# Kernel optimization log

Measured on AMD Instinct MI355X. Metric: run time of the kernel, lower is better.

The kernel has to match this reference:

```python
import jax, jax.numpy as jnp
import numpy as np

B, L, D, N_LAYERS = 128, 256, 512, 6
NEG = -9e15  # -9000000000000000.0 in the torch source


def _pair_coef(a1, L, D):
    # Faithful reduction of the torch repeat_interleave(dim=2) construction:
    # first half of a_input satisfies a_input[b, i, j, m] = h[b, i, (j*D + m)//L],
    # so sum_m a_input[...,m]*a1[m] = h[b,i] . c[j] with
    # c[j, f] = sum_{m : (j*D+m)//L == f} a1[m].
    j = jnp.arange(L)[:, None]
    m = jnp.arange(D)[None, :]
    idx = (j * D + m) // L  # [L, D], values in [0, D-1]
    c = jnp.zeros((L, D), a1.dtype)
    c = c.at[jnp.arange(L)[:, None], idx].add(jnp.broadcast_to(a1[None, :], (L, D)))
    return c


def gat_layer(x, adj, W, a):
    # h = x @ W; e[b,i,j] = relu(a_input[b,i,j,:] @ a)  (relu overwrites leakyrelu in source)
    h = x @ W  # [B, L, D]
    d = W.shape[1]
    a1, a2 = a[:d, 0], a[d:, 0]
    c = _pair_coef(a1, h.shape[1], d)  # [L, D]
    e = jax.nn.relu(jnp.einsum('bif,jf->bij', h, c) + (h @ a2)[:, None, :])
    att = jnp.where(adj > 0, e, NEG)
    att = jax.nn.softmax(att, axis=2)  # dropout is identity in eval
    h_prime = jnp.einsum('bij,bjd->bid', att, h)
    return jax.nn.elu(h_prime)  # concat=True branch


def position_weight(x, left_len, aspect_len, text_len):
    j = jnp.arange(x.shape[1])[None, :].astype(jnp.float32)  # [1, L]
    l = left_len[:, None].astype(jnp.float32)
    r = (left_len + aspect_len - 1)[:, None].astype(jnp.float32)
    tl = text_len[:, None].astype(jnp.float32)
    ctx = (text_len - aspect_len)[:, None].astype(jnp.float32)
    w = jnp.where(j < l, 1.0 - (l - j) / ctx,
        jnp.where(j <= r, 0.0,
        jnp.where(j < tl, 1.0 - (j - r) / ctx, 0.0)))
    return w[..., None].astype(x.dtype) * x


def aspect_mask(x, left_len, aspect_len):
    j = jnp.arange(x.shape[1])[None, :]
    l = left_len[:, None]
    r = (left_len + aspect_len - 1)[:, None]
    m = ((j >= l) & (j <= r)).astype(x.dtype)
    return m[..., None] * x


def setup_inputs() -> dict:
    key = jax.random.key(0)
    ks = jax.random.split(key, 6)
    x = jax.random.normal(ks[0], (B, L, D), jnp.float32)
    adj = jax.random.randint(ks[1], (B, L, L), 0, 2, jnp.int32)
    adj = adj.at[:, jnp.arange(L), jnp.arange(L)].set(1)  # self loops
    left_len = jax.random.randint(ks[2], (B,), 0, 20, jnp.int32)
    aspect_len = jax.random.randint(ks[3], (B,), 1, 6, jnp.int32)
    text_len = jnp.full((B,), L, jnp.int32)
    W_stack = jax.random.normal(ks[4], (N_LAYERS, D, D), jnp.float32) * (1.414 / np.sqrt(D))
    a_stack = jax.random.normal(ks[5], (N_LAYERS, 2 * D, 1), jnp.float32) * 0.05
    return {"x": x, "W_stack": W_stack, "a_stack": a_stack, "adj": adj,
            "left_len": left_len, "aspect_len": aspect_len, "text_len": text_len}


def reference(x, W_stack, a_stack, adj, left_len, aspect_len, text_len):
    text_out = x
    xp = position_weight(text_out, left_len, aspect_len, text_len)
    h1 = jax.nn.relu(gat_layer(xp, adj, W_stack[0], a_stack[0]))
    h1 = position_weight(h1, left_len, aspect_len, text_len)
    x_graph = jnp.zeros_like(h1)
    for i in range(1, N_LAYERS):
        x_graph = x_graph + jax.nn.relu(gat_layer(h1, adj, W_stack[i], a_stack[i]))
    x_graph = 0.2 * x_graph
    graph_mask = aspect_mask(x_graph, left_len, aspect_len)
    # hop == 1 attention pooling
    alpha_mat = jnp.einsum('bld,bmd->blm', graph_mask, text_out)  # [B, L, L]
    alpha = jax.nn.softmax(alpha_mat.sum(axis=1, keepdims=True), axis=2)  # [B, 1, L]
    a1 = jnp.einsum('blm,bmd->bld', alpha, text_out)[:, 0, :]  # [B, D]
    return a1
```

## Files before the change

kernel.cpp:

```cpp
#include <hip/hip_runtime.h>

#define NB 128
#define NLQ 256
#define ND 512
#define NLAYERS 6
#define DD (ND*ND)
#define MN (1024*ND)
#define HTB 131072

typedef _Float16 f16x8 __attribute__((ext_vector_type(8)));
typedef __fp16 fp16x2 __attribute__((ext_vector_type(2)));
typedef _Float16 f16x4v __attribute__((ext_vector_type(4)));
typedef float f32x4 __attribute__((ext_vector_type(4)));
typedef unsigned int u32x2 __attribute__((ext_vector_type(2)));
typedef unsigned int u32x4 __attribute__((ext_vector_type(4)));
typedef unsigned short ushort_t;

#define GLOAD16(gp, lp) __builtin_amdgcn_global_load_lds( \
    (const __attribute__((address_space(1))) void*)(gp), \
    (__attribute__((address_space(3))) void*)(lp), 16, 0, 0)

__device__ __forceinline__ float wave_max(float v){
  #pragma unroll
  for(int off=32; off; off>>=1) v = fmaxf(v, __shfl_xor(v, off));
  return v;
}
__device__ __forceinline__ float wave_sum(float v){
  #pragma unroll
  for(int off=32; off; off>>=1) v += __shfl_xor(v, off);
  return v;
}
__device__ __forceinline__ unsigned int pk16(float a, float b){
  fp16x2 h = __builtin_amdgcn_cvt_pkrtz(a, b);
  return __builtin_bit_cast(unsigned int, h);
}

__global__ __launch_bounds__(256) void k_scal(const float* __restrict__ a_stack,
                                              float* __restrict__ scal){
  int layer = blockIdx.x;
  const float* a = a_stack + (size_t)layer*2*ND;
  int t = threadIdx.x;
  float v0 = a[t];
  float v1 = a[256 + t];
  v0 = wave_sum(v0); v1 = wave_sum(v1);
  __shared__ float s0[4], s1[4];
  int wave = t>>6, lane = t&63;
  if(lane==0){ s0[wave]=v0; s1[wave]=v1; }
  __syncthreads();
  if(t==0){
    scal[layer*2+0] = s0[0]+s0[1]+s0[2]+s0[3];
    scal[layer*2+1] = s1[0]+s1[1]+s1[2]+s1[3];
  }
}

__global__ __launch_bounds__(256) void k_wa2(const float* __restrict__ Wst,
                                             const float* __restrict__ ast,
                                             float* __restrict__ v){
  int l  = blockIdx.x >> 7;
  int rg = blockIdx.x & 127;
  int i  = rg*4 + (threadIdx.x>>6);
  int lane = threadIdx.x & 63;
  const float4* wr = (const float4*)(Wst + (size_t)(l+1)*DD + (size_t)i*ND);
  const float4* ar = (const float4*)(ast + (size_t)(l+1)*2*ND + ND);
  float4 w0=wr[lane], w1=wr[lane+64], a0=ar[lane], a1=ar[lane+64];
  float d = w0.x*a0.x + w0.y*a0.y + w0.z*a0.z + w0.w*a0.w
          + w1.x*a1.x + w1.y*a1.y + w1.z*a1.z + w1.w*a1.w;
  d = wave_sum(d);
  if(lane==0) v[l*ND + i] = d;
}

__global__ __launch_bounds__(256) void k_wcvt(const float* __restrict__ Wsrc,
                                              ushort_t* __restrict__ Ho){
  __shared__ float CT[64][65];
  int bid = blockIdx.x;
  int l  = bid >> 6;
  int kt = (bid >> 3) & 7, nt = bid & 7;
  const float* Wl = Wsrc + (size_t)l*DD;
  int t = threadIdx.x;
  int r = t >> 2, c4 = (t&3)*16;
  #pragma unroll
  for(int u=0;u<4;u++){
    float4 vv = *(const float4*)(Wl + (size_t)(kt*64+r)*ND + nt*64 + c4 + u*4);
    CT[r][c4+u*4+0]=vv.x; CT[r][c4+u*4+1]=vv.y;
    CT[r][c4+u*4+2]=vv.z; CT[r][c4+u*4+3]=vv.w;
  }
  __syncthreads();
  int n = t >> 2, kc = t & 3;
  unsigned int o[8];
  #pragma unroll
  for(int j=0;j<8;j++)
    o[j] = pk16(CT[kc*16 + 2*j][n], CT[kc*16 + 2*j + 1][n]);
  ushort_t* dh = Ho + (size_t)l*DD + (size_t)(nt*64+n)*ND + kt*64 + kc*16;
  *(u32x4*)(dh)     = (u32x4){o[0],o[1],o[2],o[3]};
  *(u32x4*)(dh + 8) = (u32x4){o[4],o[5],o[6],o[7]};
}

#define ROWB 80
template<int MODE>
__device__ __forceinline__ void gemm_tile(const float* __restrict__ A,
                                          const ushort_t* __restrict__ Wth,
                                          float* __restrict__ C,
                                          unsigned int* __restrict__ hP,
                                          ushort_t* __restrict__ Pbuf,
                                          float* __restrict__ tp4,
                                          const float* __restrict__ a2,
                                          const float* __restrict__ scal,
                                          const int* __restrict__ left,
                                          const int* __restrict__ asp,
                                          const int* __restrict__ tl,
                                          int mtile, int ntile, unsigned char* lds){
  unsigned char* Ah = lds;
  unsigned char* Bh = lds + 128*ROWB;

  int t = threadIdx.x;
  int m0 = mtile*128, n0 = ntile*128;
  int lane = t & 63, wid = t >> 6;
  int wr = wid >> 1, wc = wid & 1;
  int lrow = lane & 15, kb = lane >> 4;

  f32x4 acc[4][4];
  #pragma unroll
  for(int mi=0;mi<4;mi++)
    #pragma unroll
    for(int ni=0;ni<4;ni++)
      acc[mi][ni] = (f32x4){0.f,0.f,0.f,0.f};

  int a_row = t >> 3;
  int a_kq  = t & 7;
  int w_n   = t >> 2;
  int w_kc  = t & 3;

  float wgt_[4] = {1.f,1.f,1.f,1.f};
  if(MODE == 1){
    int b = mtile >> 1;
    float lf=(float)left[b], aspf=(float)asp[b], tlf=(float)tl[b];
    float rr=lf+aspf-1.f, ctx=tlf-aspf;
    #pragma unroll
    for(int p=0;p<4;p++){
      float jf = (float)((mtile&1)*128 + a_row + p*32);
      float w;
      if(jf < lf)       w = 1.f-(lf-jf)/ctx;
      else if(jf <= rr) w = 0.f;
      else if(jf < tlf) w = 1.f-(jf-rr)/ctx;
      else              w = 0.f;
      wgt_[p] = w;
    }
  }

  float4 pa[4];
  u32x4 pwh[2];

  #pragma unroll
  for(int p=0;p<4;p++)
    pa[p] = *(const float4*)(A + (size_t)(m0 + a_row + p*32)*ND + a_kq*4);
  #pragma unroll
  for(int h=0;h<2;h++)
    pwh[h] = *(const u32x4*)(Wth + (size_t)(n0 + w_n + h*64)*ND + w_kc*8);

  for(int k0=0; k0<ND; k0+=32){
    #pragma unroll
    for(int p=0;p<4;p++){
      int row = a_row + p*32;
      unsigned int c0 = pk16(pa[p].x*wgt_[p], pa[p].y*wgt_[p]);
      unsigned int c1 = pk16(pa[p].z*wgt_[p], pa[p].w*wgt_[p]);
      *(u32x2*)(Ah + row*ROWB + a_kq*8) = (u32x2){c0, c1};
    }
    #pragma unroll
    for(int h=0;h<2;h++)
      *(u32x4*)(Bh + (w_n + h*64)*ROWB + w_kc*16) = pwh[h];
    __syncthreads();

    if(k0 + 32 < ND){
      int kn = k0 + 32;
      #pragma unroll
      for(int p=0;p<4;p++)
        pa[p] = *(const float4*)(A + (size_t)(m0 + a_row + p*32)*ND + kn + a_kq*4);
      #pragma unroll
      for(int h=0;h<2;h++)
        pwh[h] = *(const u32x4*)(Wth + (size_t)(n0 + w_n + h*64)*ND + kn + w_kc*8);
    }

    f16x8 ah[4], bh[4];
    #pragma unroll
    for(int mi=0;mi<4;mi++)
      ah[mi] = *(const f16x8*)(Ah + (wr*64 + mi*16 + lrow)*ROWB + kb*16);
    #pragma unroll
    for(int ni=0;ni<4;ni++)
      bh[ni] = *(const f16x8*)(Bh + (wc*64 + ni*16 + lrow)*ROWB + kb*16);

    #pragma unroll
    for(int mi=0;mi<4;mi++)
      #pragma unroll
      for(int ni=0;ni<4;ni++)
        acc[mi][ni] = __builtin_amdgcn_mfma_f32_16x16x32_f16(ah[mi], bh[ni], acc[mi][ni], 0,0,0);
    __syncthreads();
  }

  int rg = lane >> 4;
  int cc = lane & 15;
  if(MODE == 0){
    #pragma unroll
    for(int mi=0;mi<4;mi++)
      #pragma unroll
      for(int ni=0;ni<4;ni++){
        int col = n0 + wc*64 + ni*16 + cc;
        #pragma unroll
        for(int q=0;q<4;q++){
          int row = m0 + wr*64 + mi*16 + rg*4 + q;
          C[(size_t)row*ND + col] = acc[mi][ni][q];
        }
      }
  } else {
    float S0 = scal[0], S1 = scal[1];
    float* CT = (float*)lds;
    int b = m0 >> 8;
    int ibase = m0 & 255;
    int tr   = t >> 1;
    int tch  = t & 1;
    float tpsum = 0.f;
    #pragma unroll
    for(int p=0;p<2;p++){
      if(wc == p){
        #pragma unroll
        for(int mi=0;mi<4;mi++)
          #pragma unroll
          for(int ni=0;ni<4;ni++)
            #pragma unroll
            for(int q=0;q<4;q++)
              CT[(ni*16+cc)*130 + wr*64 + mi*16 + rg*4 + q] = acc[mi][ni][q];
      }
      __syncthreads();
      int lcol = t >> 6;
      int lrow2 = (t & 63)*2;
      #pragma unroll
      for(int u=0;u<16;u++){
        int c = lcol + u*4;
        float2 v2 = *(float2*)&CT[c*130 + lrow2];
        size_t uidx = ((size_t)b*HTB + (size_t)(n0 + p*64 + c)*256 + ibase + lrow2) >> 1;
        hP[uidx] = pk16(v2.x, v2.y);
      }
      {
        int cpr = t & 31;
        int rq  = t >> 5;
        #pragma unroll
        for(int rr2=0; rr2<16; rr2++){
          int row = rq*16 + rr2;
          float pval = S0*CT[(2*cpr)*130 + row] + S1*CT[(2*cpr+1)*130 + row];
          int ig = ibase + row;
          _Float16 ph = (_Float16)pval;
          size_t addr = (size_t)b*262144 + (size_t)(ig>>5)*32768
                      + (size_t)(ig&31)*256 + (n0>>1) + p*32 + cpr;
          Pbuf[addr] = __builtin_bit_cast(unsigned short, ph);
        }
      }
      #pragma unroll 8
      for(int cc2=0; cc2<32; cc2++){
        int c = tch*32 + cc2;
        tpsum = fmaf(CT[c*130 + tr], a2[n0 + p*64 + c], tpsum);
      }
      __syncthreads();
    }
    tpsum += __shfl_xor(tpsum, 1);
    if(tch == 0) tp4[(n0>>7)*32768 + m0 + tr] = tpsum;
  }
}

__global__ __launch_bounds__(256) void k_gemm_t(const float* __restrict__ A,
                                                const ushort_t* __restrict__ Wth,
                                                unsigned int* __restrict__ hP,
                                                ushort_t* __restrict__ Pbuf,
                                                float* __restrict__ tp4,
                                                const float* __restrict__ a2,
                                                const float* __restrict__ scal,
                                                const int* __restrict__ left,
                                                const int* __restrict__ asp,
                                                const int* __restrict__ tl){
  __shared__ unsigned char lds[33280];
  int bid = blockIdx.x;
  int ntile = (bid >> 3) & 3;
  int mtile = (bid & 7) | ((bid >> 5) << 3);
  gemm_tile<1>(A, Wth, nullptr, hP, Pbuf, tp4, a2, scal, left, asp, tl,
               mtile, ntile, lds);
}

__global__ __launch_bounds__(256) void k_gemm_b(const float* __restrict__ Abase, long aStride,
                                                const ushort_t* __restrict__ Wth,
                                                float* __restrict__ Cbase){
  __shared__ unsigned char lds[2*128*ROWB];
  int l  = blockIdx.x >> 5;
  int tb = blockIdx.x & 31;
  gemm_tile<0>(Abase + (size_t)l*aStride, Wth + (size_t)l*DD,
               Cbase + (size_t)l*MN, nullptr, nullptr, nullptr,
               nullptr, nullptr, nullptr, nullptr, nullptr, tb>>2, tb&3, lds);
}

__global__ __launch_bounds__(256) void k_attn0(
    const ushort_t* __restrict__ hTH,
    const int* __restrict__ adj,
    const float* __restrict__ tpart,
    const int* __restrict__ left, const int* __restrict__ asp, const int* __restrict__ tl,
    float* __restrict__ PA){
  __shared__ unsigned char attH[32*512];
  __shared__ unsigned char BsH[16384];

  int bid = blockIdx.x;
  int b  = bid & 127;
  int ic = bid >> 7;
  int i0 = ic*32;
  int tid = threadIdx.x;
  int lane = tid & 63, w = tid >> 6;
  const ushort_t* HH = hTH + (size_t)b*HTB;
  const ushort_t* Pt = (const ushort_t*)PA + (size_t)b*262144 + (size_t)ic*32768;

  float t0v=0.f, t1v=0.f, t2v=0.f, t3v=0.f;
  #pragma unroll
  for(int nt=0; nt<4; nt++){
    float4 tv = ((const float4*)(tpart + nt*32768 + b*256))[lane];
    t0v += tv.x; t1v += tv.y; t2v += tv.z; t3v += tv.w;
  }

  for(int rr=0; rr<8; rr++){
    int il = w*8 + rr;
    int i  = i0 + il;
    f16x4v pv = *(const f16x4v*)(Pt + il*256 + lane*4);
    int4 av = ((const int4*)(adj + ((size_t)b*NLQ + i)*NLQ))[lane];
    float e0 = fmaxf((float)pv[0] + t0v, 0.f);
    float e1 = fmaxf((float)pv[1] + t1v, 0.f);
    float e2 = fmaxf((float)pv[2] + t2v, 0.f);
    float e3 = fmaxf((float)pv[3] + t3v, 0.f);
    float m = -3.0e38f;
    if(av.x>0) m = e0;
    if(av.y>0) m = fmaxf(m, e1);
    if(av.z>0) m = fmaxf(m, e2);
    if(av.w>0) m = fmaxf(m, e3);
    m = wave_max(m);
    float p0 = (av.x>0) ? __expf(e0-m) : 0.f;
    float p1 = (av.y>0) ? __expf(e1-m) : 0.f;
    float p2 = (av.z>0) ? __expf(e2-m) : 0.f;
    float p3 = (av.w>0) ? __expf(e3-m) : 0.f;
    float s = wave_sum(p0+p1+p2+p3);
    float inv = 1.f/s;
    unsigned int w0 = pk16(p0*inv, p1*inv);
    unsigned int w1 = pk16(p2*inv, p3*inv);
    int off = il*512 + ((lane*8) ^ ((il&7)<<4));
    *(u32x2*)(attH + off) = (u32x2){w0,w1};
  }

  int wm = w >> 1, wn = w & 1;
  int lrow = lane & 15, kb = lane >> 4;
  int rg = lane >> 4, cc = lane & 15;
  float lf=(float)left[b], aspf=(float)asp[b], tlf=(float)tl[b];
  float rrv=lf+aspf-1.f, ctx=tlf-aspf;
  int arow = wm*16 + lrow;
  int aswz = (arow&7)<<4;

  for(int dp=0; dp<2; dp++){
    int d0 = dp*256;
    f32x4 acc[8];
    #pragma unroll
    for(int ni=0;ni<8;ni++) acc[ni] = (f32x4){0.f,0.f,0.f,0.f};
    for(int ks=0; ks<8; ks++){
      int j0 = ks*32;
      __syncthreads();
      #pragma unroll
      for(int u=0;u<4;u++){
        int chunk = (u*4 + w)*64 + lane;
        int row = chunk >> 2, sl = chunk & 3;
        GLOAD16(HH + (size_t)(d0+row)*256 + j0 + sl*8, BsH + (u*4+w)*1024);
      }
      __syncthreads();
      int aoff = arow*512 + ((j0*2 + kb*16) ^ aswz);
      f16x8 ah = *(const f16x8*)(attH + aoff);
      #pragma unroll
      for(int ni=0; ni<8; ni++){
        f16x8 bh = *(const f16x8*)(BsH + (wn*128 + ni*16 + lrow)*64 + kb*16);
        acc[ni] = __builtin_amdgcn_mfma_f32_16x16x32_f16(ah, bh, acc[ni], 0,0,0);
      }
    }
    #pragma unroll
    for(int q=0;q<4;q++){
      int row = i0 + wm*16 + rg*4 + q;
      float fi = (float)row;
      float wgt;
      if(fi < lf)        wgt = 1.f-(lf-fi)/ctx;
      else if(fi <= rrv) wgt = 0.f;
      else if(fi < tlf)  wgt = 1.f-(fi-rrv)/ctx;
      else               wgt = 0.f;
      #pragma unroll
      for(int ni=0;ni<8;ni++){
        int col = d0 + wn*128 + ni*16 + cc;
        PA[((size_t)b*NLQ + row)*ND + col] = wgt*fmaxf(acc[ni][q], 0.f);
      }
    }
  }
}

__global__ __launch_bounds__(256) void k_tv(const float* __restrict__ h1,
                                            const float* __restrict__ v,
                                            float* __restrict__ T){
  int row  = blockIdx.x*4 + (threadIdx.x>>6);
  int lane = threadIdx.x & 63;
  const float4* hr = (const float4*)(h1 + (size_t)row*ND);
  float4 h0 = hr[lane], h1v = hr[lane+64];
  float s0,s1,s2,s3,s4;
  #define DOTV(SL, L) { \
    const float4* vr = (const float4*)(v + (L)*ND); \
    float4 v0 = vr[lane], v1 = vr[lane+64]; \
    float dd = h0.x*v0.x+h0.y*v0.y+h0.z*v0.z+h0.w*v0.w \
             + h1v.x*v1.x+h1v.y*v1.y+h1v.z*v1.z+h1v.w*v1.w; \
    SL = wave_sum(dd); }
  DOTV(s0,0) DOTV(s1,1) DOTV(s2,2) DOTV(s3,3) DOTV(s4,4)
  #undef DOTV
  if(lane==0){
    T[0*32768 + row]=s0; T[1*32768 + row]=s1; T[2*32768 + row]=s2;
    T[3*32768 + row]=s3; T[4*32768 + row]=s4;
  }
}

__global__ __launch_bounds__(256) void k_rows(const float* __restrict__ h1,
                                              const int* __restrict__ left, const int* __restrict__ asp,
                                              float* __restrict__ R){
  int b = blockIdx.x;
  int nk = asp[b], l0 = left[b];
  const float4* src = (const float4*)(h1 + (size_t)b*NLQ*ND);
  float4* dst = (float4*)(R + (size_t)b*8*ND);
  #pragma unroll
  for(int u=0; u<4; u++){
    int f4 = threadIdx.x + u*256;
    int k = f4 >> 7, c = f4 & 127;
    float4 val = (k<nk) ? src[(size_t)(l0+k)*128 + c] : (float4){0.f,0.f,0.f,0.f};
    dst[f4] = val;
  }
}

__global__ __launch_bounds__(256) void k_att5(const float* __restrict__ h1,
    const float* __restrict__ Hasp, const float* __restrict__ T,
    const int* __restrict__ adj, const float* __restrict__ scal,
    const int* __restrict__ left, const int* __restrict__ asp,
    float* __restrict__ y){
  __shared__ float att[25][260];
  int b  = blockIdx.x & 127;
  int dh = blockIdx.x >> 7;
  int tid = threadIdx.x, lane = tid&63, w = tid>>6;
  int nk = asp[b], l0 = left[b];

  for(int r = w; r < 25; r += 4){
    int l = r/5, k = r - l*5;
    if(k < nk){
      float S0 = scal[2*(l+1)], S1 = scal[2*(l+1)+1];
      const float2* hrow = (const float2*)(Hasp + (size_t)l*MN + (size_t)(b*8+k)*ND);
      const int* arow = adj + ((size_t)b*NLQ + (l0+k))*NLQ;
      const float* Tl = T + l*32768 + b*256;
      float e[4]; int av[4];
      float m = -3.0e38f;
      #pragma unroll
      for(int q=0;q<4;q++){
        int j = lane + 64*q;
        float2 hp = hrow[j];
        av[q] = arow[j];
        e[q] = fmaxf(S0*hp.x + S1*hp.y + Tl[j], 0.f);
        if(av[q] > 0) m = fmaxf(m, e[q]);
      }
      m = wave_max(m);
      float pp[4]; float s = 0.f;
      #pragma unroll
      for(int q=0;q<4;q++){
        pp[q] = (av[q] > 0) ? __expf(e[q]-m) : 0.f;
        s += pp[q];
      }
      s = wave_sum(s);
      float inv = 1.f/s;
      #pragma unroll
      for(int q=0;q<4;q++) att[r][lane+64*q] = pp[q]*inv;
    } else {
      #pragma unroll
      for(int q=0;q<4;q++) att[r][lane+64*q] = 0.f;
    }
  }
  __syncthreads();

  int d = dh*256 + tid;
  const float* hb = h1 + (size_t)b*NLQ*ND;
  float acc[25];
  #pragma unroll
  for(int r=0;r<25;r++) acc[r]=0.f;
  for(int jj=0; jj<NLQ; jj++){
    float hv = hb[(size_t)jj*ND + d];
    #pragma unroll
    for(int r=0;r<25;r++) acc[r] += att[r][jj]*hv;
  }
  #pragma unroll
  for(int r=0;r<25;r++){
    int l = r/5, k = r - l*5;
    y[(size_t)l*MN + ((size_t)b*8+k)*ND + d] = acc[r];
  }
  #pragma unroll
  for(int l=0;l<5;l++)
    #pragma unroll
    for(int k=5;k<8;k++)
      y[(size_t)l*MN + ((size_t)b*8+k)*ND + d] = 0.f;
}

__global__ __launch_bounds__(256) void k_g(const float* __restrict__ hp,
    const int* __restrict__ asp, float* __restrict__ g){
  int b = blockIdx.x, d = threadIdx.x;
  int nk = asp[b];
  float gx=0.f, gy=0.f;
  for(int l=0;l<5;l++){
    for(int k=0;k<nk;k++){
      const float* r = hp + (size_t)l*MN + (size_t)(b*8+k)*ND;
      gx += fmaxf(r[d], 0.f);
      gy += fmaxf(r[d+256], 0.f);
    }
  }
  g[b*ND + d]       = 0.2f*gx;
  g[b*ND + 256 + d] = 0.2f*gy;
}

__global__ __launch_bounds__(256) void k_dot(const float* __restrict__ x,
    const float* __restrict__ g, float* __restrict__ s){
  int row  = blockIdx.x*4 + (threadIdx.x>>6);
  int b    = row >> 8;
  int lane = threadIdx.x & 63;
  const float4* xr = (const float4*)(x + (size_t)row*ND);
  const float4* gr = (const float4*)(g + (size_t)b*ND);
  float4 x0=xr[lane], x1=xr[lane+64], g0=gr[lane], g1=gr[lane+64];
  float d = x0.x*g0.x + x0.y*g0.y + x0.z*g0.z + x0.w*g0.w
          + x1.x*g1.x + x1.y*g1.y + x1.z*g1.z + x1.w*g1.w;
  d = wave_sum(d);
  if(lane==0) s[row] = d;
}

__global__ __launch_bounds__(256) void k_out(const float* __restrict__ x,
    const float* __restrict__ s, float* __restrict__ out){
  int b  = blockIdx.x >> 2;
  int ch = blockIdx.x & 3;
  int tid = threadIdx.x, lane = tid&63, w = tid>>6;
  __shared__ float red[4];
  __shared__ float alpha[NLQ];
  __shared__ float part[128];
  float sv = s[b*NLQ + tid];
  float m = wave_max(sv);
  if(lane==0) red[w] = m;
  __syncthreads();
  m = fmaxf(fmaxf(red[0],red[1]), fmaxf(red[2],red[3]));
  float p = __expf(sv - m);
  float su = wave_sum(p);
  __syncthreads();
  if(lane==0) red[w] = su;
  __syncthreads();
  su = red[0]+red[1]+red[2]+red[3];
  alpha[tid] = p/su;
  __syncthreads();
  int d = ch*128 + (tid & 127);
  int half = tid >> 7;
  const float* xb = x + (size_t)b*NLQ*ND;
  float acc = 0.f;
  for(int mm = half*128; mm < half*128 + 128; mm++)
    acc += alpha[mm] * xb[(size_t)mm*ND + d];
  if(half) part[tid & 127] = acc;
  __syncthreads();
  if(!half) out[(size_t)b*ND + d] = acc + part[tid & 127];
}

extern "C" void kernel_launch(void* const* d_in, const int* in_sizes, int n_in,
                              void* d_out, int out_size, void* d_ws, size_t ws_size,
                              hipStream_t stream){
  const float* x    = (const float*)d_in[0];
  const float* Wst  = (const float*)d_in[1];
  const float* ast  = (const float*)d_in[2];
  const int*   adj  = (const int*)d_in[3];
  const int*   left = (const int*)d_in[4];
  const int*   asp  = (const int*)d_in[5];
  const int*   tl   = (const int*)d_in[6];
  float* out = (float*)d_out;
  float* ws  = (float*)d_ws;

  const size_t SZ = (size_t)NB*NLQ*ND;
  float* bufA = ws;
  float* bufB = ws + SZ;
  float* ws2  = ws + 2*SZ;
  float* tpart= ws2;
  float* T    = tpart + 4*32768;
  float* g    = T + 163840;
  float* scal = g + 65536;
  float* v    = scal + 16;
  float* sbuf = v + 2560;
  ushort_t* w0th = (ushort_t*)(sbuf + 32768);

  ushort_t* hTH = (ushort_t*)bufB;

  float* Hasp = bufB;
  float* ybuf = Hasp + (size_t)5*MN;
  float* hp   = ybuf + (size_t)5*MN;
  float* R    = hp   + (size_t)5*MN;
  ushort_t* wt15h = (ushort_t*)(R + MN);

  k_scal<<<NLAYERS, 256, 0, stream>>>(ast, scal);
  k_wa2<<<5*128, 256, 0, stream>>>(Wst, ast, v);
  k_wcvt<<<64, 256, 0, stream>>>(Wst, w0th);

  k_gemm_t<<<(NB*NLQ/128)*(ND/128), 256, 0, stream>>>(x, w0th,
      (unsigned int*)hTH, (ushort_t*)bufA, tpart, ast + ND, scal, left, asp, tl);
  k_attn0<<<NB*8, 256, 0, stream>>>(hTH, adj, tpart, left, asp, tl, bufA);

  k_wcvt<<<5*64, 256, 0, stream>>>(Wst + DD, wt15h);
  k_tv<<<NB*NLQ/4, 256, 0, stream>>>(bufA, v, T);
  k_rows<<<NB, 256, 0, stream>>>(bufA, left, asp, R);
  k_gemm_b<<<5*32, 256, 0, stream>>>(R, 0L, wt15h, Hasp);
  k_att5<<<NB*2, 256, 0, stream>>>(bufA, Hasp, T, adj, scal, left, asp, ybuf);
  k_gemm_b<<<5*32, 256, 0, stream>>>(ybuf, (long)MN, wt15h, hp);
  k_g<<<NB, 256, 0, stream>>>(hp, asp, g);

  k_dot<<<NB*NLQ/4, 256, 0, stream>>>(x, g, sbuf);
  k_out<<<NB*4, 256, 0, stream>>>(x, sbuf, out);
}
```

Measured before the change: 253.0 us.

## Split k_att5 grid by layer instead of feature half

The aspect-row attention kernel now launches one block per (batch, layer) instead of per (batch, feature half). Each block builds softmax rows for only its layer's up-to-5 aspect rows and covers all 512 features, two per thread. The grid grows from 256 to 640 blocks for better occupancy on the many CUs, and per-thread accumulators drop from 25 to 10. In exchange, h1 is re-read once per layer instead of once per feature half, which raises global traffic.

```diff
diff --git a/kernel.cpp b/kernel.cpp
--- a/kernel.cpp
+++ b/kernel.cpp
@@ -438,16 +438,15 @@
     const int* __restrict__ adj, const float* __restrict__ scal,
     const int* __restrict__ left, const int* __restrict__ asp,
     float* __restrict__ y){
-  __shared__ float att[25][260];
+  __shared__ float att[5][260];
   int b  = blockIdx.x & 127;
-  int dh = blockIdx.x >> 7;
+  int l  = blockIdx.x >> 7;
   int tid = threadIdx.x, lane = tid&63, w = tid>>6;
   int nk = asp[b], l0 = left[b];
-
-  for(int r = w; r < 25; r += 4){
-    int l = r/5, k = r - l*5;
+  float S0 = scal[2*(l+1)], S1 = scal[2*(l+1)+1];
+
+  for(int k = w; k < 5; k += 4){
     if(k < nk){
-      float S0 = scal[2*(l+1)], S1 = scal[2*(l+1)+1];
       const float2* hrow = (const float2*)(Hasp + (size_t)l*MN + (size_t)(b*8+k)*ND);
       const int* arow = adj + ((size_t)b*NLQ + (l0+k))*NLQ;
       const float* Tl = T + l*32768 + b*256;
@@ -471,34 +470,35 @@
       s = wave_sum(s);
       float inv = 1.f/s;
       #pragma unroll
-      for(int q=0;q<4;q++) att[r][lane+64*q] = pp[q]*inv;
+      for(int q=0;q<4;q++) att[k][lane+64*q] = pp[q]*inv;
     } else {
       #pragma unroll
-      for(int q=0;q<4;q++) att[r][lane+64*q] = 0.f;
-    }
-  }
-  __syncthreads();
-
-  int d = dh*256 + tid;
+      for(int q=0;q<4;q++) att[k][lane+64*q] = 0.f;
+    }
+  }
+  __syncthreads();
+
+  int d = tid;
   const float* hb = h1 + (size_t)b*NLQ*ND;
-  float acc[25];
-  #pragma unroll
-  for(int r=0;r<25;r++) acc[r]=0.f;
+  float ax[5] = {0,0,0,0,0}, ay[5] = {0,0,0,0,0};
   for(int jj=0; jj<NLQ; jj++){
-    float hv = hb[(size_t)jj*ND + d];
-    #pragma unroll
-    for(int r=0;r<25;r++) acc[r] += att[r][jj]*hv;
-  }
-  #pragma unroll
-  for(int r=0;r<25;r++){
-    int l = r/5, k = r - l*5;
-    y[(size_t)l*MN + ((size_t)b*8+k)*ND + d] = acc[r];
-  }
-  #pragma unroll
-  for(int l=0;l<5;l++)
-    #pragma unroll
-    for(int k=5;k<8;k++)
-      y[(size_t)l*MN + ((size_t)b*8+k)*ND + d] = 0.f;
+    float hx = hb[(size_t)jj*ND + d];
+    float hy = hb[(size_t)jj*ND + 256 + d];
+    #pragma unroll
+    for(int k=0;k<5;k++){
+      float a = att[k][jj];
+      ax[k] += a*hx;
+      ay[k] += a*hy;
+    }
+  }
+  float* yb = y + (size_t)l*MN + (size_t)b*8*ND;
+  #pragma unroll
+  for(int k=0;k<5;k++){
+    yb[(size_t)k*ND + d]       = ax[k];
+    yb[(size_t)k*ND + 256 + d] = ay[k];
+  }
+  #pragma unroll
+  for(int u=0;u<6;u++) yb[5*ND + u*256 + tid] = 0.f;
 }
 
 __global__ __launch_bounds__(256) void k_g(const float* __restrict__ hp,
@@ -608,7 +608,7 @@
   k_tv<<<NB*NLQ/4, 256, 0, stream>>>(bufA, v, T);
   k_rows<<<NB, 256, 0, stream>>>(bufA, left, asp, R);
   k_gemm_b<<<5*32, 256, 0, stream>>>(R, 0L, wt15h, Hasp);
-  k_att5<<<NB*2, 256, 0, stream>>>(bufA, Hasp, T, adj, scal, left, asp, ybuf);
+  k_att5<<<5*NB, 256, 0, stream>>>(bufA, Hasp, T, adj, scal, left, asp, ybuf);
   k_gemm_b<<<5*32, 256, 0, stream>>>(ybuf, (long)MN, wt15h, hp);
   k_g<<<NB, 256, 0, stream>>>(hp, asp, g);
 
```

New measurement: 215.4 us. -14.9%, faster.
